# Kernel tuning notes

Measured on AMD Instinct MI355X. Metric: run time of the kernel, lower is better.

## Reference

```python
import jax, jax.numpy as jnp
import numpy as np
import math

WINDOW = 512
N_HEAD = 16

def setup_inputs() -> dict:
    key = jax.random.key(0)
    ks = jax.random.split(key, 5)
    B, L, D = 2, 4096, 1024
    s = 0.02
    return {
        "x": jax.random.normal(ks[0], (B, L, D), dtype=jnp.float32),
        "Wq": jax.random.normal(ks[1], (D, D), dtype=jnp.float32) * s,
        "bq": jnp.zeros((D,), jnp.float32),
        "Wk": jax.random.normal(ks[2], (D, D), dtype=jnp.float32) * s,
        "bk": jnp.zeros((D,), jnp.float32),
        "Wv": jax.random.normal(ks[3], (D, D), dtype=jnp.float32) * s,
        "bv": jnp.zeros((D,), jnp.float32),
        "Wo": jax.random.normal(ks[4], (D, D), dtype=jnp.float32) * s,
        "bo": jnp.zeros((D,), jnp.float32),
    }

def reference(x, Wq, bq, Wk, bk, Wv, bv, Wo, bo):
    # Chunked sliding-window MHA (eval mode, dropout inactive).
    B, L, D = x.shape
    W, H = WINDOW, N_HEAD
    dh = D // H
    C = L // W  # number of query chunks
    scale = 1.0 / math.sqrt(dh)

    # Project full sequence once (linear, per-token -> identical math).
    q = x @ Wq.T + bq
    k = x @ Wk.T + bk
    v = x @ Wv.T + bv

    # Pad K/V by one window at the front so every chunk sees 2W keys.
    kp = jnp.pad(k, ((0, 0), (W, 0), (0, 0)))
    vp = jnp.pad(v, ((0, 0), (W, 0), (0, 0)))
    idx = jnp.arange(C)[:, None] * W + jnp.arange(2 * W)[None, :]  # [C, 2W] into padded seq
    kc = kp[:, idx].reshape(B, C, 2 * W, H, dh)
    vc = vp[:, idx].reshape(B, C, 2 * W, H, dh)
    qc = q.reshape(B, C, W, H, dh)

    scores = jnp.einsum('bcqhd,bckhd->bchqk', qc, kc) * scale  # [B,C,H,W,2W]
    valid = (idx >= W)  # padded positions (chunk 0's lookback) are invalid
    scores = jnp.where(valid[None, :, None, None, :], scores, jnp.float32(-1e9))
    attn = jax.nn.softmax(scores, axis=-1)
    out = jnp.einsum('bchqk,bckhd->bcqhd', attn, vc).reshape(B, L, D)
    return out @ Wo.T + bo
```

## Files before the change

### kernel.cpp

```cpp
#include <hip/hip_runtime.h>
#include <hip/hip_bf16.h>

typedef __hip_bfloat16 bf16;
typedef __attribute__((ext_vector_type(8))) short bf16x8;
typedef __attribute__((ext_vector_type(4))) float f32x4;
typedef unsigned int u32;
typedef unsigned short u16;

#define MFMA(a,b,c) __builtin_amdgcn_mfma_f32_16x16x32_bf16((a),(b),(c),0,0,0)

__device__ __forceinline__ u16 f32_to_bf16_rtne(float f) {
  u32 b = __builtin_bit_cast(u32, f);
  b += 0x7FFFu + ((b >> 16) & 1u);
  return (u16)(b >> 16);
}
__device__ __forceinline__ float bf16_to_f32(u16 h) {
  return __builtin_bit_cast(float, (u32)h << 16);
}
__device__ __forceinline__ u32 pk2bf(float a, float b) {
  u32 ua = __builtin_bit_cast(u32, a); ua += 0x7FFFu + ((ua >> 16) & 1u);
  u32 ub = __builtin_bit_cast(u32, b); ub += 0x7FFFu + ((ub >> 16) & 1u);
  return __builtin_amdgcn_perm(ub, ua, 0x07060302u);
}
__device__ __forceinline__ u32 pk2bf_rtz(float a, float b) {
  return __builtin_amdgcn_perm(__builtin_bit_cast(u32, b),
                               __builtin_bit_cast(u32, a), 0x07060302u);
}

__device__ __forceinline__ void barrier_lgkm() {
  asm volatile("s_waitcnt lgkmcnt(0)\n\ts_barrier" ::: "memory");
}

static constexpr float SL2E = 0.125f * 1.44269504f;

__global__ void detect_mode(const u16* __restrict__ x_raw, int* __restrict__ flag) {
  __shared__ int cnt;
  if (threadIdx.x == 0) cnt = 0;
  __syncthreads();
  int ok = 0;
  for (int i = threadIdx.x; i < 1024; i += 256) {
    const int e = (x_raw[2 * i] >> 7) & 0xFF;
    if (e >= 117 && e <= 137) ok++;
  }
  atomicAdd(&cnt, ok);
  __syncthreads();
  if (threadIdx.x == 0) *flag = (cnt < 512) ? 1 : 0;
}

__device__ __forceinline__ void cast8(const void* src, u16* dst, int mode, size_t i) {
  union { u16 h[8]; uint4 v; } u;
  if (mode) {
    const float4* s = (const float4*)src + i * 2;
    const float4 a = s[0], b = s[1];
    u.h[0] = f32_to_bf16_rtne(a.x); u.h[1] = f32_to_bf16_rtne(a.y);
    u.h[2] = f32_to_bf16_rtne(a.z); u.h[3] = f32_to_bf16_rtne(a.w);
    u.h[4] = f32_to_bf16_rtne(b.x); u.h[5] = f32_to_bf16_rtne(b.y);
    u.h[6] = f32_to_bf16_rtne(b.z); u.h[7] = f32_to_bf16_rtne(b.w);
  } else {
    u.v = ((const uint4*)src)[i];
  }
  ((uint4*)dst)[i] = u.v;
}

__global__ __launch_bounds__(256)
void cast_all(const void* __restrict__ x,
              const void* __restrict__ wq, const void* __restrict__ wk,
              const void* __restrict__ wv, const void* __restrict__ wo,
              u16* __restrict__ xb, u16* __restrict__ wqkv,
              u16* __restrict__ wob, const int* __restrict__ flag) {
  const int mode = *flag;
  const int bid = blockIdx.x;
  if (bid < 4096) {
    cast8(x, xb, mode, (size_t)bid * 256 + threadIdx.x);
  } else {
    const size_t DD8 = (size_t)1024 * 1024 / 8;
    const int m = (bid - 4096) >> 9;
    const size_t i = ((size_t)((bid - 4096) & 511)) * 256 + threadIdx.x;
    const void* src = (m == 0) ? wq : (m == 1) ? wk : (m == 2) ? wv : wo;
    u16* dst = (m < 3) ? (wqkv + (size_t)m * DD8 * 8) : wob;
    cast8(src, dst, mode, i);
  }
}

template <int MODE>
__global__ __launch_bounds__(256)
void gemm_bt(const bf16* __restrict__ A, const bf16* __restrict__ W,
             const void* __restrict__ b0, const void* __restrict__ b1,
             const void* __restrict__ b2, void* __restrict__ o0,
             void* __restrict__ o1, void* __restrict__ o2,
             const int* __restrict__ flag, int M, int N, int K)
{
  __shared__ bf16 As[128 * 64];
  __shared__ bf16 Bs[128 * 64];

  const int mode = *flag;
  const int tid  = threadIdx.x;
  const int wave = tid >> 6, lane = tid & 63;
  const int quad = lane >> 4, l16 = lane & 15;
  const int wm   = wave >> 1, wn  = wave & 1;
  const int m0   = blockIdx.x * 128, n0 = blockIdx.y * 128;

  const int band = n0 >> 10;
  const void* bias = (band == 0) ? b0 : (band == 1) ? b1 : b2;

  const int srow = lane >> 3;
  const int sg   = lane & 7;
  const size_t rgs = (size_t)8 * K;
  const bf16* aSrc = A + (size_t)(m0 + wave * 32 + srow) * K + sg * 8;
  const bf16* wSrc = W + (size_t)(n0 + wave * 32 + srow) * K + sg * 8;
  bf16* aDst = As + (wave * 32 + srow) * 64 + ((sg ^ srow) * 8);
  bf16* wDst = Bs + (wave * 32 + srow) * 64 + ((sg ^ srow) * 8);

  const int niter = K >> 6;

  uint4 a0 = *(const uint4*)(aSrc);
  uint4 a1 = *(const uint4*)(aSrc + rgs);
  uint4 a2 = *(const uint4*)(aSrc + 2 * rgs);
  uint4 a3 = *(const uint4*)(aSrc + 3 * rgs);
  uint4 w0 = *(const uint4*)(wSrc);
  uint4 w1 = *(const uint4*)(wSrc + rgs);
  uint4 w2 = *(const uint4*)(wSrc + 2 * rgs);
  uint4 w3 = *(const uint4*)(wSrc + 3 * rgs);
  aSrc += 64; wSrc += 64;

  f32x4 acc[4][4] = {};

  const int arow[4] = { (wm * 64 + 0 * 16 + l16) * 64, (wm * 64 + 1 * 16 + l16) * 64,
                        (wm * 64 + 2 * 16 + l16) * 64, (wm * 64 + 3 * 16 + l16) * 64 };
  const int brow[4] = { (wn * 64 + 0 * 16 + l16) * 64, (wn * 64 + 1 * 16 + l16) * 64,
                        (wn * 64 + 2 * 16 + l16) * 64, (wn * 64 + 3 * 16 + l16) * 64 };
  const int r7 = l16 & 7;

  for (int t = 0; t < niter; ++t) {
    if (t) barrier_lgkm();
    *(uint4*)(aDst)        = a0;
    *(uint4*)(aDst + 512)  = a1;
    *(uint4*)(aDst + 1024) = a2;
    *(uint4*)(aDst + 1536) = a3;
    *(uint4*)(wDst)        = w0;
    *(uint4*)(wDst + 512)  = w1;
    *(uint4*)(wDst + 1024) = w2;
    *(uint4*)(wDst + 1536) = w3;
    barrier_lgkm();
    if (t + 1 < niter) {
      a0 = *(const uint4*)(aSrc);
      a1 = *(const uint4*)(aSrc + rgs);
      a2 = *(const uint4*)(aSrc + 2 * rgs);
      a3 = *(const uint4*)(aSrc + 3 * rgs);
      w0 = *(const uint4*)(wSrc);
      w1 = *(const uint4*)(wSrc + rgs);
      w2 = *(const uint4*)(wSrc + 2 * rgs);
      w3 = *(const uint4*)(wSrc + 3 * rgs);
      aSrc += 64; wSrc += 64;
    }
#pragma unroll
    for (int kk = 0; kk < 2; ++kk) {
      bf16x8 af[4], bw[4];
#pragma unroll
      for (int mt = 0; mt < 4; ++mt)
        af[mt] = *(const bf16x8*)(As + arow[mt] + (((kk * 4 + quad) ^ r7) * 8));
#pragma unroll
      for (int nt = 0; nt < 4; ++nt)
        bw[nt] = *(const bf16x8*)(Bs + brow[nt] + (((kk * 4 + quad) ^ r7) * 8));
#pragma unroll
      for (int mt = 0; mt < 4; ++mt)
#pragma unroll
        for (int nt = 0; nt < 4; ++nt)
          acc[mt][nt] = MFMA(af[mt], bw[nt], acc[mt][nt]);
    }
  }

#pragma unroll
  for (int nt = 0; nt < 4; ++nt) {
    const int col = n0 + wn * 64 + nt * 16 + l16;
    const int cl  = col & 1023;
    const float bv = mode ? ((const float*)bias)[cl]
                          : bf16_to_f32(((const u16*)bias)[cl]);
#pragma unroll
    for (int mt = 0; mt < 4; ++mt) {
      const int rbase = m0 + wm * 64 + mt * 16 + quad * 4;
      if (MODE == 1) {
#pragma unroll
        for (int r = 0; r < 4; ++r) {
          const float val = acc[mt][nt][r] + bv;
          const size_t idx = (size_t)(rbase + r) * N + col;
          if (mode) ((float*)o0)[idx] = val;
          else      ((u16*)o0)[idx]   = f32_to_bf16_rtne(val);
        }
      } else if (band == 2) {
        const int hh = cl >> 6, dd = cl & 63;
        const int bb = rbase >> 12, tl = rbase & 4095;
        u16* dst = (u16*)o2 + ((size_t)((bb * 16 + hh) * 64 + dd)) * 4096 + tl;
        uint2 pk;
        pk.x = pk2bf(acc[mt][nt][0] + bv, acc[mt][nt][1] + bv);
        pk.y = pk2bf(acc[mt][nt][2] + bv, acc[mt][nt][3] + bv);
        *(uint2*)dst = pk;
      } else {
        u16* dst = (u16*)((band == 0) ? o0 : o1);
        const float sc = (band == 0) ? SL2E : 1.0f;
#pragma unroll
        for (int r = 0; r < 4; ++r)
          dst[(size_t)(rbase + r) * 1024 + cl] =
              f32_to_bf16_rtne((acc[mt][nt][r] + bv) * sc);
      }
    }
  }
}

__global__ __launch_bounds__(256)
void attn_swin(const bf16* __restrict__ qb, const bf16* __restrict__ kb,
               const bf16* __restrict__ vtb, u16* __restrict__ ctx)
{
  __shared__ __align__(16) bf16 Ks[2][64 * 72];
  __shared__ __align__(16) bf16 Vts[2][64 * 72];

  int bid = blockIdx.x;
  const int g  = bid & 255, qt = bid >> 8;
  const int h  = g & 15, c = (g >> 4) & 7, b = g >> 7;

  const int tid  = threadIdx.x;
  const int w    = tid >> 6, lane = tid & 63;
  const int quad = lane >> 4, l16 = lane & 15;

  const int tq0  = c * 512 + qt * 128;
  const int hoff = h * 64;
  const int kstart = (c == 0) ? 0 : (c - 1) * 512;
  const int nkt    = (c == 0) ? 8 : 16;

  bf16x8 qf[2][2];
#pragma unroll
  for (int u = 0; u < 2; ++u) {
    const bf16* qr = qb + ((size_t)(b * 4096 + tq0 + w * 32 + u * 16 + l16)) * 1024 + hoff;
    qf[u][0] = *(const bf16x8*)(qr + quad * 8);
    qf[u][1] = *(const bf16x8*)(qr + 32 + quad * 8);
  }

  const int m    = tid >> 2;
  const int cseg = (tid & 3) * 16;
  const int sig  = (((m >> 4) & 1) << 5) | (((m >> 2) & 3) << 3)
                 | (((m >> 5) & 1) << 2) | (m & 3);
  const bf16* kgp = kb + ((size_t)(b * 4096 + kstart + sig)) * 1024 + hoff + cseg;
  const bf16* vgp = vtb + ((size_t)((b * 16 + h) * 64 + m)) * 4096 + kstart + cseg;
  const int soff = m * 72 + cseg;

  float l_i[2] = {0.f, 0.f};
  f32x4 o[2][4] = {};

  uint4 ka0 = *(const uint4*)(kgp), ka1 = *(const uint4*)(kgp + 8);
  uint4 va0 = *(const uint4*)(vgp), va1 = *(const uint4*)(vgp + 8);
  kgp += (size_t)64 * 1024; vgp += 64;
  *(uint4*)(Ks[0] + soff) = ka0; *(uint4*)(Ks[0] + soff + 8) = ka1;
  *(uint4*)(Vts[0] + soff) = va0; *(uint4*)(Vts[0] + soff + 8) = va1;
  ka0 = *(const uint4*)(kgp); ka1 = *(const uint4*)(kgp + 8);
  va0 = *(const uint4*)(vgp); va1 = *(const uint4*)(vgp + 8);
  kgp += (size_t)64 * 1024; vgp += 64;
  barrier_lgkm();

  typedef union { u32 d[4]; bf16x8 v; } fragu;

  auto compute = [&](const bf16* ksb, const bf16* vtsb) {
    f32x4 s[2][4] = {};
#pragma unroll
    for (int kt = 0; kt < 4; ++kt) {
      const bf16* kr = ksb + (kt * 16 + l16) * 72;
      bf16x8 kf0 = *(const bf16x8*)(kr + quad * 8);
      bf16x8 kf1 = *(const bf16x8*)(kr + 32 + quad * 8);
      s[0][kt] = MFMA(kf0, qf[0][0], s[0][kt]);
      s[0][kt] = MFMA(kf1, qf[0][1], s[0][kt]);
      s[1][kt] = MFMA(kf0, qf[1][0], s[1][kt]);
      s[1][kt] = MFMA(kf1, qf[1][1], s[1][kt]);
    }
    fragu pf[2][2];
#pragma unroll
    for (int u = 0; u < 2; ++u) {
      float rs = 0.f;
#pragma unroll
      for (int kt = 0; kt < 4; ++kt)
#pragma unroll
        for (int r = 0; r < 4; ++r) {
          const float p = __builtin_amdgcn_exp2f(s[u][kt][r]);
          s[u][kt][r] = p;
          rs += p;
        }
      rs += __shfl_xor(rs, 16);
      rs += __shfl_xor(rs, 32);
      l_i[u] += rs;
#pragma unroll
      for (int hh = 0; hh < 2; ++hh)
#pragma unroll
        for (int dw = 0; dw < 4; ++dw) {
          const int kt = 2 * (dw >> 1) + hh, r0 = 2 * (dw & 1);
          pf[u][hh].d[dw] = pk2bf_rtz(s[u][kt][r0], s[u][kt][r0 + 1]);
        }
    }
#pragma unroll
    for (int dt = 0; dt < 4; ++dt) {
      const bf16* vr = vtsb + (dt * 16 + l16) * 72;
      bf16x8 vf0 = *(const bf16x8*)(vr + quad * 8);
      bf16x8 vf1 = *(const bf16x8*)(vr + 32 + quad * 8);
      o[0][dt] = MFMA(vf0, pf[0][0].v, o[0][dt]);
      o[0][dt] = MFMA(vf1, pf[0][1].v, o[0][dt]);
      o[1][dt] = MFMA(vf0, pf[1][0].v, o[1][dt]);
      o[1][dt] = MFMA(vf1, pf[1][1].v, o[1][dt]);
    }
  };

  for (int t = 0; t < nkt; t += 2) {
    *(uint4*)(Ks[1] + soff) = ka0; *(uint4*)(Ks[1] + soff + 8) = ka1;
    *(uint4*)(Vts[1] + soff) = va0; *(uint4*)(Vts[1] + soff + 8) = va1;
    if (t + 2 < nkt) {
      ka0 = *(const uint4*)(kgp); ka1 = *(const uint4*)(kgp + 8);
      va0 = *(const uint4*)(vgp); va1 = *(const uint4*)(vgp + 8);
      kgp += (size_t)64 * 1024; vgp += 64;
    }
    compute(Ks[0], Vts[0]);
    barrier_lgkm();

    if (t + 2 < nkt) {
      *(uint4*)(Ks[0] + soff) = ka0; *(uint4*)(Ks[0] + soff + 8) = ka1;
      *(uint4*)(Vts[0] + soff) = va0; *(uint4*)(Vts[0] + soff + 8) = va1;
      if (t + 3 < nkt) {
        ka0 = *(const uint4*)(kgp); ka1 = *(const uint4*)(kgp + 8);
        va0 = *(const uint4*)(vgp); va1 = *(const uint4*)(vgp + 8);
        kgp += (size_t)64 * 1024; vgp += 64;
      }
    }
    compute(Ks[1], Vts[1]);
    barrier_lgkm();
  }

#pragma unroll
  for (int u = 0; u < 2; ++u) {
    const float inv = 1.0f / l_i[u];
    const int qrow = tq0 + w * 32 + u * 16 + l16;
    u16* crow = ctx + ((size_t)(b * 4096 + qrow)) * 1024 + hoff;
#pragma unroll
    for (int dt = 0; dt < 4; ++dt) {
      uint2 pk;
      pk.x = pk2bf(o[u][dt][0] * inv, o[u][dt][1] * inv);
      pk.y = pk2bf(o[u][dt][2] * inv, o[u][dt][3] * inv);
      *(uint2*)(crow + dt * 16 + quad * 4) = pk;
    }
  }
}

extern "C" void kernel_launch(void* const* d_in, const int* in_sizes, int n_in,
                              void* d_out, int out_size, void* d_ws, size_t ws_size,
                              hipStream_t stream) {
  const void* x  = d_in[0];
  const void* Wq = d_in[1];
  const void* bq = d_in[2];
  const void* Wk = d_in[3];
  const void* bk = d_in[4];
  const void* Wv = d_in[5];
  const void* bv = d_in[6];
  const void* Wo = d_in[7];
  const void* bo = d_in[8];

  const size_t MD = (size_t)8192 * 1024;
  const size_t DD = (size_t)1024 * 1024;

  char* ws = (char*)d_ws;
  int*  flag  = (int*)ws;                     ws += 256;
  u16*  xb    = (u16*)ws;                     ws += MD * 2;
  u16*  Wqkvb = (u16*)ws;                     ws += 3 * DD * 2;
  u16*  Wob   = (u16*)ws;                     ws += DD * 2;
  u16*  qbuf  = (u16*)ws;                     ws += MD * 2;
  u16*  kbuf  = (u16*)ws;                     ws += MD * 2;
  u16*  vtb   = (u16*)ws;                     ws += MD * 2;
  u16*  ctx   = (u16*)ws;

  detect_mode<<<dim3(1), dim3(256), 0, stream>>>((const u16*)x, flag);
  cast_all<<<dim3(6144), dim3(256), 0, stream>>>(x, Wq, Wk, Wv, Wo,
                                                 xb, Wqkvb, Wob, flag);

  gemm_bt<0><<<dim3(64, 24), dim3(256), 0, stream>>>(
      (const bf16*)xb, (const bf16*)Wqkvb, bq, bk, bv,
      qbuf, kbuf, vtb, flag, 8192, 3072, 1024);

  attn_swin<<<dim3(1024), dim3(256), 0, stream>>>(
      (const bf16*)qbuf, (const bf16*)kbuf, (const bf16*)vtb, ctx);

  gemm_bt<1><<<dim3(64, 8), dim3(256), 0, stream>>>(
      (const bf16*)ctx, (const bf16*)Wob, bo, bo, bo,
      d_out, nullptr, nullptr, flag, 8192, 1024, 1024);
}
```

Measured before the change: 238.6 us.

## Fuse fp32-to-bf16 cast of x into QKV GEMM and drop runtime dtype detection

The QKV GEMM now reads fp32 x directly and converts each tile to bf16 while staging it into shared memory, which removes the separate cast pass over x and its bf16 workspace buffer. The dtype-detection kernel and the runtime mode flag are removed, so inputs are assumed to be fp32 and weights get a smaller dedicated cast kernel. This saves one kernel launch and one write-plus-read of x. In exchange the GEMM reads twice as many bytes of A per tile from global memory and spends extra ALU on packing.

After: 235.8 us. No clear change (-1.1%).

```diff
diff --git a/kernel.cpp b/kernel.cpp
--- a/kernel.cpp
+++ b/kernel.cpp
@@ -14,9 +14,6 @@
   b += 0x7FFFu + ((b >> 16) & 1u);
   return (u16)(b >> 16);
 }
-__device__ __forceinline__ float bf16_to_f32(u16 h) {
-  return __builtin_bit_cast(float, (u32)h << 16);
-}
 __device__ __forceinline__ u32 pk2bf(float a, float b) {
   u32 ua = __builtin_bit_cast(u32, a); ua += 0x7FFFu + ((ua >> 16) & 1u);
   u32 ub = __builtin_bit_cast(u32, b); ub += 0x7FFFu + ((ub >> 16) & 1u);
@@ -26,6 +23,14 @@
   return __builtin_amdgcn_perm(__builtin_bit_cast(u32, b),
                                __builtin_bit_cast(u32, a), 0x07060302u);
 }
+__device__ __forceinline__ uint4 cvt8(uint4 lo, uint4 hi) {
+  const float4 fl = __builtin_bit_cast(float4, lo);
+  const float4 fh = __builtin_bit_cast(float4, hi);
+  uint4 r;
+  r.x = pk2bf(fl.x, fl.y); r.y = pk2bf(fl.z, fl.w);
+  r.z = pk2bf(fh.x, fh.y); r.w = pk2bf(fh.z, fh.w);
+  return r;
+}
 
 __device__ __forceinline__ void barrier_lgkm() {
   asm volatile("s_waitcnt lgkmcnt(0)\n\ts_barrier" ::: "memory");
@@ -33,67 +38,31 @@
 
 static constexpr float SL2E = 0.125f * 1.44269504f;
 
-__global__ void detect_mode(const u16* __restrict__ x_raw, int* __restrict__ flag) {
-  __shared__ int cnt;
-  if (threadIdx.x == 0) cnt = 0;
-  __syncthreads();
-  int ok = 0;
-  for (int i = threadIdx.x; i < 1024; i += 256) {
-    const int e = (x_raw[2 * i] >> 7) & 0xFF;
-    if (e >= 117 && e <= 137) ok++;
-  }
-  atomicAdd(&cnt, ok);
-  __syncthreads();
-  if (threadIdx.x == 0) *flag = (cnt < 512) ? 1 : 0;
-}
-
-__device__ __forceinline__ void cast8(const void* src, u16* dst, int mode, size_t i) {
-  union { u16 h[8]; uint4 v; } u;
-  if (mode) {
-    const float4* s = (const float4*)src + i * 2;
-    const float4 a = s[0], b = s[1];
-    u.h[0] = f32_to_bf16_rtne(a.x); u.h[1] = f32_to_bf16_rtne(a.y);
-    u.h[2] = f32_to_bf16_rtne(a.z); u.h[3] = f32_to_bf16_rtne(a.w);
-    u.h[4] = f32_to_bf16_rtne(b.x); u.h[5] = f32_to_bf16_rtne(b.y);
-    u.h[6] = f32_to_bf16_rtne(b.z); u.h[7] = f32_to_bf16_rtne(b.w);
-  } else {
-    u.v = ((const uint4*)src)[i];
-  }
-  ((uint4*)dst)[i] = u.v;
-}
-
 __global__ __launch_bounds__(256)
-void cast_all(const void* __restrict__ x,
-              const void* __restrict__ wq, const void* __restrict__ wk,
-              const void* __restrict__ wv, const void* __restrict__ wo,
-              u16* __restrict__ xb, u16* __restrict__ wqkv,
-              u16* __restrict__ wob, const int* __restrict__ flag) {
-  const int mode = *flag;
-  const int bid = blockIdx.x;
-  if (bid < 4096) {
-    cast8(x, xb, mode, (size_t)bid * 256 + threadIdx.x);
-  } else {
-    const size_t DD8 = (size_t)1024 * 1024 / 8;
-    const int m = (bid - 4096) >> 9;
-    const size_t i = ((size_t)((bid - 4096) & 511)) * 256 + threadIdx.x;
-    const void* src = (m == 0) ? wq : (m == 1) ? wk : (m == 2) ? wv : wo;
-    u16* dst = (m < 3) ? (wqkv + (size_t)m * DD8 * 8) : wob;
-    cast8(src, dst, mode, i);
-  }
-}
-
-template <int MODE>
+void cast_w(const float* __restrict__ wq, const float* __restrict__ wk,
+            const float* __restrict__ wv, const float* __restrict__ wo,
+            u16* __restrict__ wqkv, u16* __restrict__ wob) {
+  const size_t DD8 = (size_t)1024 * 1024 / 8;
+  const int m = blockIdx.x >> 9;
+  const size_t i = ((size_t)(blockIdx.x & 511)) * 256 + threadIdx.x;
+  const float* src = (m == 0) ? wq : (m == 1) ? wk : (m == 2) ? wv : wo;
+  u16* dst = (m < 3) ? (wqkv + (size_t)m * DD8 * 8) : wob;
+  const float4* s = (const float4*)src + i * 2;
+  uint4 v = cvt8(__builtin_bit_cast(uint4, s[0]), __builtin_bit_cast(uint4, s[1]));
+  ((uint4*)dst)[i] = v;
+}
+
+template <int MODE, int CASTA>
 __global__ __launch_bounds__(256)
-void gemm_bt(const bf16* __restrict__ A, const bf16* __restrict__ W,
-             const void* __restrict__ b0, const void* __restrict__ b1,
-             const void* __restrict__ b2, void* __restrict__ o0,
+void gemm_bt(const void* __restrict__ Asrc, const bf16* __restrict__ W,
+             const float* __restrict__ b0, const float* __restrict__ b1,
+             const float* __restrict__ b2, void* __restrict__ o0,
              void* __restrict__ o1, void* __restrict__ o2,
-             const int* __restrict__ flag, int M, int N, int K)
+             int M, int N, int K)
 {
   __shared__ bf16 As[128 * 64];
   __shared__ bf16 Bs[128 * 64];
 
-  const int mode = *flag;
   const int tid  = threadIdx.x;
   const int wave = tid >> 6, lane = tid & 63;
   const int quad = lane >> 4, l16 = lane & 15;
@@ -101,27 +70,39 @@
   const int m0   = blockIdx.x * 128, n0 = blockIdx.y * 128;
 
   const int band = n0 >> 10;
-  const void* bias = (band == 0) ? b0 : (band == 1) ? b1 : b2;
+  const float* bias = (band == 0) ? b0 : (band == 1) ? b1 : b2;
 
   const int srow = lane >> 3;
   const int sg   = lane & 7;
   const size_t rgs = (size_t)8 * K;
-  const bf16* aSrc = A + (size_t)(m0 + wave * 32 + srow) * K + sg * 8;
-  const bf16* wSrc = W + (size_t)(n0 + wave * 32 + srow) * K + sg * 8;
+  const bf16*  aSrcH = (const bf16*)Asrc  + (size_t)(m0 + wave * 32 + srow) * K + sg * 8;
+  const float* aSrcF = (const float*)Asrc + (size_t)(m0 + wave * 32 + srow) * K + sg * 8;
+  const bf16*  wSrc  = W + (size_t)(n0 + wave * 32 + srow) * K + sg * 8;
   bf16* aDst = As + (wave * 32 + srow) * 64 + ((sg ^ srow) * 8);
   bf16* wDst = Bs + (wave * 32 + srow) * 64 + ((sg ^ srow) * 8);
 
   const int niter = K >> 6;
 
-  uint4 a0 = *(const uint4*)(aSrc);
-  uint4 a1 = *(const uint4*)(aSrc + rgs);
-  uint4 a2 = *(const uint4*)(aSrc + 2 * rgs);
-  uint4 a3 = *(const uint4*)(aSrc + 3 * rgs);
+  uint4 a0, a1, a2, a3;
+  uint4 a0h, a1h, a2h, a3h;
+  if (CASTA) {
+    a0 = *(const uint4*)(aSrcF);            a0h = *(const uint4*)(aSrcF + 4);
+    a1 = *(const uint4*)(aSrcF + rgs);      a1h = *(const uint4*)(aSrcF + rgs + 4);
+    a2 = *(const uint4*)(aSrcF + 2 * rgs);  a2h = *(const uint4*)(aSrcF + 2 * rgs + 4);
+    a3 = *(const uint4*)(aSrcF + 3 * rgs);  a3h = *(const uint4*)(aSrcF + 3 * rgs + 4);
+    aSrcF += 64;
+  } else {
+    a0 = *(const uint4*)(aSrcH);
+    a1 = *(const uint4*)(aSrcH + rgs);
+    a2 = *(const uint4*)(aSrcH + 2 * rgs);
+    a3 = *(const uint4*)(aSrcH + 3 * rgs);
+    aSrcH += 64;
+  }
   uint4 w0 = *(const uint4*)(wSrc);
   uint4 w1 = *(const uint4*)(wSrc + rgs);
   uint4 w2 = *(const uint4*)(wSrc + 2 * rgs);
   uint4 w3 = *(const uint4*)(wSrc + 3 * rgs);
-  aSrc += 64; wSrc += 64;
+  wSrc += 64;
 
   f32x4 acc[4][4] = {};
 
@@ -133,25 +114,41 @@
 
   for (int t = 0; t < niter; ++t) {
     if (t) barrier_lgkm();
-    *(uint4*)(aDst)        = a0;
-    *(uint4*)(aDst + 512)  = a1;
-    *(uint4*)(aDst + 1024) = a2;
-    *(uint4*)(aDst + 1536) = a3;
+    if (CASTA) {
+      *(uint4*)(aDst)        = cvt8(a0, a0h);
+      *(uint4*)(aDst + 512)  = cvt8(a1, a1h);
+      *(uint4*)(aDst + 1024) = cvt8(a2, a2h);
+      *(uint4*)(aDst + 1536) = cvt8(a3, a3h);
+    } else {
+      *(uint4*)(aDst)        = a0;
+      *(uint4*)(aDst + 512)  = a1;
+      *(uint4*)(aDst + 1024) = a2;
+      *(uint4*)(aDst + 1536) = a3;
+    }
     *(uint4*)(wDst)        = w0;
     *(uint4*)(wDst + 512)  = w1;
     *(uint4*)(wDst + 1024) = w2;
     *(uint4*)(wDst + 1536) = w3;
     barrier_lgkm();
     if (t + 1 < niter) {
-      a0 = *(const uint4*)(aSrc);
-      a1 = *(const uint4*)(aSrc + rgs);
-      a2 = *(const uint4*)(aSrc + 2 * rgs);
-      a3 = *(const uint4*)(aSrc + 3 * rgs);
+      if (CASTA) {
+        a0 = *(const uint4*)(aSrcF);            a0h = *(const uint4*)(aSrcF + 4);
+        a1 = *(const uint4*)(aSrcF + rgs);      a1h = *(const uint4*)(aSrcF + rgs + 4);
+        a2 = *(const uint4*)(aSrcF + 2 * rgs);  a2h = *(const uint4*)(aSrcF + 2 * rgs + 4);
+        a3 = *(const uint4*)(aSrcF + 3 * rgs);  a3h = *(const uint4*)(aSrcF + 3 * rgs + 4);
+        aSrcF += 64;
+      } else {
+        a0 = *(const uint4*)(aSrcH);
+        a1 = *(const uint4*)(aSrcH + rgs);
+        a2 = *(const uint4*)(aSrcH + 2 * rgs);
+        a3 = *(const uint4*)(aSrcH + 3 * rgs);
+        aSrcH += 64;
+      }
       w0 = *(const uint4*)(wSrc);
       w1 = *(const uint4*)(wSrc + rgs);
       w2 = *(const uint4*)(wSrc + 2 * rgs);
       w3 = *(const uint4*)(wSrc + 3 * rgs);
-      aSrc += 64; wSrc += 64;
+      wSrc += 64;
     }
 #pragma unroll
     for (int kk = 0; kk < 2; ++kk) {
@@ -174,19 +171,14 @@
   for (int nt = 0; nt < 4; ++nt) {
     const int col = n0 + wn * 64 + nt * 16 + l16;
     const int cl  = col & 1023;
-    const float bv = mode ? ((const float*)bias)[cl]
-                          : bf16_to_f32(((const u16*)bias)[cl]);
+    const float bv = bias[cl];
 #pragma unroll
     for (int mt = 0; mt < 4; ++mt) {
       const int rbase = m0 + wm * 64 + mt * 16 + quad * 4;
       if (MODE == 1) {
 #pragma unroll
-        for (int r = 0; r < 4; ++r) {
-          const float val = acc[mt][nt][r] + bv;
-          const size_t idx = (size_t)(rbase + r) * N + col;
-          if (mode) ((float*)o0)[idx] = val;
-          else      ((u16*)o0)[idx]   = f32_to_bf16_rtne(val);
-        }
+        for (int r = 0; r < 4; ++r)
+          ((float*)o0)[(size_t)(rbase + r) * N + col] = acc[mt][nt][r] + bv;
       } else if (band == 2) {
         const int hh = cl >> 6, dd = cl & 63;
         const int bb = rbase >> 12, tl = rbase & 4095;
@@ -347,22 +339,20 @@
 extern "C" void kernel_launch(void* const* d_in, const int* in_sizes, int n_in,
                               void* d_out, int out_size, void* d_ws, size_t ws_size,
                               hipStream_t stream) {
-  const void* x  = d_in[0];
-  const void* Wq = d_in[1];
-  const void* bq = d_in[2];
-  const void* Wk = d_in[3];
-  const void* bk = d_in[4];
-  const void* Wv = d_in[5];
-  const void* bv = d_in[6];
-  const void* Wo = d_in[7];
-  const void* bo = d_in[8];
+  const float* x  = (const float*)d_in[0];
+  const float* Wq = (const float*)d_in[1];
+  const float* bq = (const float*)d_in[2];
+  const float* Wk = (const float*)d_in[3];
+  const float* bk = (const float*)d_in[4];
+  const float* Wv = (const float*)d_in[5];
+  const float* bv = (const float*)d_in[6];
+  const float* Wo = (const float*)d_in[7];
+  const float* bo = (const float*)d_in[8];
 
   const size_t MD = (size_t)8192 * 1024;
   const size_t DD = (size_t)1024 * 1024;
 
   char* ws = (char*)d_ws;
-  int*  flag  = (int*)ws;                     ws += 256;
-  u16*  xb    = (u16*)ws;                     ws += MD * 2;
   u16*  Wqkvb = (u16*)ws;                     ws += 3 * DD * 2;
   u16*  Wob   = (u16*)ws;                     ws += DD * 2;
   u16*  qbuf  = (u16*)ws;                     ws += MD * 2;
@@ -370,18 +360,14 @@
   u16*  vtb   = (u16*)ws;                     ws += MD * 2;
   u16*  ctx   = (u16*)ws;
 
-  detect_mode<<<dim3(1), dim3(256), 0, stream>>>((const u16*)x, flag);
-  cast_all<<<dim3(6144), dim3(256), 0, stream>>>(x, Wq, Wk, Wv, Wo,
-                                                 xb, Wqkvb, Wob, flag);
-
-  gemm_bt<0><<<dim3(64, 24), dim3(256), 0, stream>>>(
-      (const bf16*)xb, (const bf16*)Wqkvb, bq, bk, bv,
-      qbuf, kbuf, vtb, flag, 8192, 3072, 1024);
+  cast_w<<<dim3(2048), dim3(256), 0, stream>>>(Wq, Wk, Wv, Wo, Wqkvb, Wob);
+
+  gemm_bt<0, 1><<<dim3(64, 24), dim3(256), 0, stream>>>(
+      x, (const bf16*)Wqkvb, bq, bk, bv, qbuf, kbuf, vtb, 8192, 3072, 1024);
 
   attn_swin<<<dim3(1024), dim3(256), 0, stream>>>(
       (const bf16*)qbuf, (const bf16*)kbuf, (const bf16*)vtb, ctx);
 
-  gemm_bt<1><<<dim3(64, 8), dim3(256), 0, stream>>>(
-      (const bf16*)ctx, (const bf16*)Wob, bo, bo, bo,
-      d_out, nullptr, nullptr, flag, 8192, 1024, 1024);
-}
+  gemm_bt<1, 0><<<dim3(64, 8), dim3(256), 0, stream>>>(
+      ctx, (const bf16*)Wob, bo, bo, bo, d_out, nullptr, nullptr, 8192, 1024, 1024);
+}
```
